# Kernel tuning notes

Measured on AMD Instinct MI355X. Metric: run time of the kernel, lower is better.

The kernel has to match this reference:

```python
import jax, jax.numpy as jnp
import numpy as np

N = 50000
E = 800000
D = 128          # in_dim = hid_dim = out_dim
R = 8            # num_rels
B = 8            # num_bases
N_LAYERS = 2


def _rgcn_conv(x, basis, comp, root, bias, src, dst, etype):
    """One PyG-style RGCNConv with basis decomposition, mean aggregation per
    relation, root (self-loop) weight and bias.
    x: [N, Din]; basis: [B, Din, Dout]; comp: [R, B]; root: [Din, Dout]; bias: [Dout].
    """
    n = x.shape[0]
    # Relation weights from basis decomposition: W[r] = sum_b comp[r,b] * basis[b]
    W = jnp.einsum('rb,bio->rio', comp, basis)           # [R, Din, Dout]
    # Transform every node under every relation, then gather per-edge message.
    H = jnp.einsum('ni,rio->nro', x, W)                  # [N, R, Dout]
    msg = H[src, etype]                                  # [E, Dout]
    # Per-(dst, relation) in-degree for mean aggregation (PyG aggr='mean').
    deg = jnp.zeros((n, R), x.dtype).at[dst, etype].add(1.0)
    inv = 1.0 / jnp.maximum(deg[dst, etype], 1.0)        # [E]
    agg = jnp.zeros((n, W.shape[2]), x.dtype).at[dst].add(msg * inv[:, None])
    return agg + x @ root + bias


def setup_inputs() -> dict:
    key = jax.random.key(0)
    ks = jax.random.split(key, 3 + 4 * N_LAYERS)
    x = jax.random.normal(ks[0], (N, D), dtype=jnp.float32)
    edge_index = jax.random.randint(ks[1], (2, E), 0, N, dtype=jnp.int64)
    edge_type = jax.random.randint(ks[2], (E,), 0, R, dtype=jnp.int64)
    inp = {'x': x, 'edge_index': edge_index, 'edge_type': edge_type}
    scale = 1.0 / np.sqrt(D)
    for l in range(N_LAYERS):
        k0, k1, k2 = ks[3 + 4 * l], ks[4 + 4 * l], ks[5 + 4 * l]
        inp[f'basis{l}'] = jax.random.normal(k0, (B, D, D), dtype=jnp.float32) * scale
        inp[f'comp{l}'] = jax.random.normal(k1, (R, B), dtype=jnp.float32) * (1.0 / np.sqrt(B))
        inp[f'root{l}'] = jax.random.normal(k2, (D, D), dtype=jnp.float32) * scale
        inp[f'bias{l}'] = jnp.zeros((D,), dtype=jnp.float32)
    return inp


def reference(x, edge_index, edge_type,
              basis0, comp0, root0, bias0,
              basis1, comp1, root1, bias1):
    src, dst = edge_index[0], edge_index[1]
    etype = edge_type
    h = _rgcn_conv(x, basis0, comp0, root0, bias0, src, dst, etype)
    h = jax.nn.relu(h)                 # activation between layers (dropout=0.0)
    h = _rgcn_conv(h, basis1, comp1, root1, bias1, src, dst, etype)
    return h
```

## Files before the change

### kernel.cpp

```cpp
#include <hip/hip_runtime.h>

#define NN 50000
#define EE 800000
#define DD 128
#define RR 8
#define SLOTS 9
#define KSTACK 1152
#define NR2 (NN * RR)
#define GRPB 32
#define STROW 304
#define STW (GRPB * STROW)

typedef __attribute__((ext_vector_type(8))) short bf16x8;
typedef __attribute__((ext_vector_type(4))) float f32x4;

__device__ inline float bf2f(ushort u) {
    union { uint i; float f; } v; v.i = ((uint)u) << 16; return v.f;
}
__device__ inline ushort f2bf(float f) {
    uint b = __float_as_uint(f);
    uint r = (b + 0x7fffu + ((b >> 16) & 1u)) >> 16;
    return (ushort)r;
}

__global__ void __launch_bounds__(256) k_build_w4(
        const float* __restrict__ b0, const float* __restrict__ c0,
        const float* __restrict__ r0, const float* __restrict__ b1,
        const float* __restrict__ c1, const float* __restrict__ r1,
        ushort* __restrict__ w0, ushort* __restrict__ w1) {
    __shared__ float tile[32][132];
    const float* basis = blockIdx.y ? b1 : b0;
    const float* comp  = blockIdx.y ? c1 : c0;
    const float* root  = blockIdx.y ? r1 : r0;
    ushort* wT         = blockIdx.y ? w1 : w0;
    int tid = threadIdx.x;
    int k0 = blockIdx.x * 32;
    #pragma unroll
    for (int it = 0; it < 16; ++it) {
        int idx = it * 256 + tid;
        int kk = idx >> 7, o = idx & 127;
        int k = k0 + kk;
        float val;
        if (k < RR * DD) {
            int r = k >> 7, i = k & 127;
            float s = 0.f;
            #pragma unroll
            for (int b = 0; b < 8; ++b) s += comp[r * 8 + b] * basis[(b * 128 + i) * 128 + o];
            val = s;
        } else {
            val = root[(k - RR * DD) * 128 + o];
        }
        tile[kk][o] = val;
    }
    __syncthreads();
    int o = tid >> 1, half = tid & 1;
    int s = k0 >> 7, i0 = k0 & 127;
    ushort* wp = wT + ((size_t)(s * 128 + o)) * 128 + i0 + half * 16;
    #pragma unroll
    for (int j = 0; j < 8; ++j) {
        float lo = tile[half * 16 + 2 * j][o];
        float hi = tile[half * 16 + 2 * j + 1][o];
        uint pk;
        asm("v_cvt_pk_bf16_f32 %0, %1, %2" : "=v"(pk) : "v"(lo), "v"(hi));
        *(uint*)(wp + 2 * j) = pk;
    }
}

__global__ void k_hist(const int* __restrict__ ei, const int* __restrict__ et,
                       int* __restrict__ deg_dr, int* __restrict__ row_cnt) {
    int e = blockIdx.x * 256 + threadIdx.x;
    if (e < EE) {
        int d = ei[EE + e], t = et[e];
        atomicAdd(&deg_dr[d * RR + t], 1);
        atomicAdd(&row_cnt[d], 1);
    }
}

__global__ void k_scan1(const int* __restrict__ cnt, int* __restrict__ bsum, int n) {
    __shared__ int s[256];
    int t = threadIdx.x;
    int i = blockIdx.x * 256 + t;
    s[t] = (i < n) ? cnt[i] : 0;
    __syncthreads();
    for (int o = 128; o > 0; o >>= 1) {
        if (t < o) s[t] += s[t + o];
        __syncthreads();
    }
    if (t == 0) bsum[blockIdx.x] = s[0];
}

__global__ void k_scan2(int* __restrict__ bsum, int nb) {
    __shared__ int s[256];
    int t = threadIdx.x;
    int v = (t < nb) ? bsum[t] : 0;
    s[t] = v;
    __syncthreads();
    for (int o = 1; o < 256; o <<= 1) {
        int u = (t >= o) ? s[t - o] : 0;
        __syncthreads();
        s[t] += u;
        __syncthreads();
    }
    if (t < nb) bsum[t] = s[t] - v;
}

__global__ void k_scan3(const int* __restrict__ cnt, const int* __restrict__ boff,
                        int* __restrict__ ptr, int n) {
    __shared__ int s[256];
    int t = threadIdx.x;
    int i = blockIdx.x * 256 + t;
    int v = (i < n) ? cnt[i] : 0;
    s[t] = v;
    __syncthreads();
    for (int o = 1; o < 256; o <<= 1) {
        int u = (t >= o) ? s[t - o] : 0;
        __syncthreads();
        s[t] += u;
        __syncthreads();
    }
    if (i < n) ptr[i + 1] = boff[blockIdx.x] + s[t];
    if (i == 0) ptr[0] = 0;
}

__global__ void k_scatter(const int* __restrict__ ei, const int* __restrict__ et,
                          const int* __restrict__ row_ptr, const int* __restrict__ deg_dr,
                          int* __restrict__ cursor, int2* __restrict__ ekw) {
    int e = blockIdx.x * 256 + threadIdx.x;
    if (e < EE) {
        int s = ei[e], d = ei[EE + e], t = et[e];
        int p = row_ptr[d] + atomicAdd(&cursor[d], 1);
        int2 pk;
        pk.x = s * SLOTS + t;
        pk.y = __float_as_int(1.f / (float)deg_dr[d * RR + t]);
        ekw[p] = pk;
    }
}

__global__ void __launch_bounds__(512, 2) k_gemmH3(
        const float* __restrict__ Af32, const ushort* __restrict__ Abf,
        const ushort* __restrict__ BT, ushort* __restrict__ H) {
    __shared__ char lds[8 * STW];
    char* atb = lds;
    int tid = threadIdx.x, wid = tid >> 6, lane = tid & 63;
    int blockrow = blockIdx.x * GRPB;

    {
        int row = tid >> 4, seg = tid & 15;
        int gr = blockrow + row; if (gr > NN - 1) gr = NN - 1;
        uint4 pk;
        if (Af32) {
            const float4* sp = (const float4*)(Af32 + (size_t)gr * DD + seg * 8);
            float4 v0 = sp[0], v1 = sp[1];
            asm("v_cvt_pk_bf16_f32 %0, %1, %2" : "=v"(pk.x) : "v"(v0.x), "v"(v0.y));
            asm("v_cvt_pk_bf16_f32 %0, %1, %2" : "=v"(pk.y) : "v"(v0.z), "v"(v0.w));
            asm("v_cvt_pk_bf16_f32 %0, %1, %2" : "=v"(pk.z) : "v"(v1.x), "v"(v1.y));
            asm("v_cvt_pk_bf16_f32 %0, %1, %2" : "=v"(pk.w) : "v"(v1.z), "v"(v1.w));
        } else {
            pk = *(const uint4*)(Abf + (size_t)gr * DD + seg * 8);
        }
        uint off = (uint)(row * 256) + (((uint)seg * 16) ^ ((uint)(row & 7) << 4));
        *(uint4*)(atb + off) = pk;
    }
    __syncthreads();

    int rlo = lane & 15, q = lane >> 4;
    int colw = wid * 144;
    f32x4 acc[2][9];
    #pragma unroll
    for (int f = 0; f < 2; ++f)
        #pragma unroll
        for (int c = 0; c < 9; ++c) acc[f][c] = (f32x4){0.f, 0.f, 0.f, 0.f};

    const ushort* bp = BT + (size_t)(colw + rlo) * DD + q * 8;
    uint x7 = (uint)(rlo & 7) << 4;
    #pragma unroll
    for (int kk = 0; kk < 4; ++kk) {
        uint loff = ((uint)(kk * 64 + q * 16)) ^ x7;
        bf16x8 a0 = *(const bf16x8*)(atb + rlo * 256 + loff);
        bf16x8 a1 = *(const bf16x8*)(atb + (rlo + 16) * 256 + loff);
        #pragma unroll
        for (int c = 0; c < 9; ++c) {
            bf16x8 b = *(const bf16x8*)(bp + (size_t)c * 16 * DD + kk * 32);
            acc[0][c] = __builtin_amdgcn_mfma_f32_16x16x32_bf16(a0, b, acc[0][c], 0, 0, 0);
            acc[1][c] = __builtin_amdgcn_mfma_f32_16x16x32_bf16(a1, b, acc[1][c], 0, 0, 0);
        }
    }
    __syncthreads();

    char* stb = lds + wid * STW;
    #pragma unroll
    for (int f = 0; f < 2; ++f) {
        #pragma unroll
        for (int c = 0; c < 9; ++c) {
            #pragma unroll
            for (int rg = 0; rg < 4; ++rg) {
                int r = f * 16 + q * 4 + rg;
                *(ushort*)(stb + r * STROW + (c * 16 + rlo) * 2) = f2bf(acc[f][c][rg]);
            }
        }
    }
    #pragma unroll
    for (int k = 0; k < 9; ++k) {
        int ci = k * 64 + lane;
        int r = (int)(((uint)ci * 58255u) >> 20);
        int j = ci - r * 18;
        int row = blockrow + r;
        if (row < NN) {
            uint4 v = *(const uint4*)(stb + r * STROW + j * 16);
            *(uint4*)(H + (size_t)row * KSTACK + colw + j * 8) = v;
        }
    }
}

__global__ void __launch_bounds__(256) k_agg2(const ushort* __restrict__ H,
                                              const int* __restrict__ row_ptr,
                                              const int2* __restrict__ ekw,
                                              const float* __restrict__ bias,
                                              ushort* __restrict__ hout,
                                              float* __restrict__ fout) {
    int wid = threadIdx.x >> 6, lane = threadIdx.x & 63;
    int n = blockIdx.x * 4 + wid;
    int l2 = lane << 1;
    uint su = *(const uint*)(H + ((size_t)n * SLOTS + RR) * DD + l2);
    float a0 = bf2f((ushort)(su & 0xffffu));
    float a1 = bf2f((ushort)(su >> 16));
    int p = row_ptr[n], p1 = row_ptr[n + 1];
    for (; p + 4 <= p1; p += 4) {
        int2 e0 = ekw[p], e1 = ekw[p + 1], e2 = ekw[p + 2], e3 = ekw[p + 3];
        uint u0 = *(const uint*)(H + (size_t)e0.x * DD + l2);
        uint u1 = *(const uint*)(H + (size_t)e1.x * DD + l2);
        uint u2 = *(const uint*)(H + (size_t)e2.x * DD + l2);
        uint u3 = *(const uint*)(H + (size_t)e3.x * DD + l2);
        float w0 = __int_as_float(e0.y), w1 = __int_as_float(e1.y);
        float w2 = __int_as_float(e2.y), w3 = __int_as_float(e3.y);
        a0 += w0 * bf2f((ushort)(u0 & 0xffffu)) + w1 * bf2f((ushort)(u1 & 0xffffu))
            + w2 * bf2f((ushort)(u2 & 0xffffu)) + w3 * bf2f((ushort)(u3 & 0xffffu));
        a1 += w0 * bf2f((ushort)(u0 >> 16)) + w1 * bf2f((ushort)(u1 >> 16))
            + w2 * bf2f((ushort)(u2 >> 16)) + w3 * bf2f((ushort)(u3 >> 16));
    }
    for (; p < p1; ++p) {
        int2 e = ekw[p];
        uint u = *(const uint*)(H + (size_t)e.x * DD + l2);
        float w = __int_as_float(e.y);
        a0 += w * bf2f((ushort)(u & 0xffffu));
        a1 += w * bf2f((ushort)(u >> 16));
    }
    a0 += bias[l2];
    a1 += bias[l2 + 1];
    if (hout) {
        a0 = fmaxf(a0, 0.f);
        a1 = fmaxf(a1, 0.f);
        *(uint*)(hout + (size_t)n * DD + l2) = (uint)f2bf(a0) | ((uint)f2bf(a1) << 16);
    } else {
        float2 v; v.x = a0; v.y = a1;
        *(float2*)(fout + (size_t)n * DD + l2) = v;
    }
}

extern "C" void kernel_launch(void* const* d_in, const int* in_sizes, int n_in,
                              void* d_out, int out_size, void* d_ws, size_t ws_size,
                              hipStream_t stream) {
    const float* x      = (const float*)d_in[0];
    const int*   ei     = (const int*)d_in[1];
    const int*   et     = (const int*)d_in[2];
    const float* basis0 = (const float*)d_in[3];
    const float* comp0  = (const float*)d_in[4];
    const float* root0  = (const float*)d_in[5];
    const float* bias0  = (const float*)d_in[6];
    const float* basis1 = (const float*)d_in[7];
    const float* comp1  = (const float*)d_in[8];
    const float* root1  = (const float*)d_in[9];
    const float* bias1  = (const float*)d_in[10];
    float* out = (float*)d_out;

    char* ws = (char*)d_ws;
    size_t off = 0;
    auto alloc = [&](size_t bytes) -> void* {
        void* p = ws + off;
        off += (bytes + 255) & ~(size_t)255;
        return p;
    };
    int*    deg_dr  = (int*)alloc((size_t)NR2 * 4);
    int*    row_cnt = (int*)alloc((size_t)NN * 4);
    int*    cursor  = (int*)alloc((size_t)NN * 4);
    size_t zero_bytes = off;
    int*    row_ptr = (int*)alloc((size_t)(NN + 1) * 4);
    int*    bsum    = (int*)alloc(256 * 4);
    int2*   ekw     = (int2*)alloc((size_t)EE * 8);
    ushort* BT0     = (ushort*)alloc((size_t)KSTACK * DD * 2);
    ushort* BT1     = (ushort*)alloc((size_t)KSTACK * DD * 2);
    ushort* h       = (ushort*)alloc((size_t)NN * DD * 2);
    ushort* H       = (ushort*)alloc((size_t)NN * KSTACK * 2);
    if (off > ws_size) return;

    hipMemsetAsync(d_ws, 0, zero_bytes, stream);

    dim3 wgrid(KSTACK / 32, 2);
    k_build_w4<<<wgrid, 256, 0, stream>>>(basis0, comp0, root0, basis1, comp1, root1, BT0, BT1);
    k_hist<<<3125, 256, 0, stream>>>(ei, et, deg_dr, row_cnt);
    k_scan1<<<196, 256, 0, stream>>>(row_cnt, bsum, NN);
    k_scan2<<<1, 256, 0, stream>>>(bsum, 196);
    k_scan3<<<196, 256, 0, stream>>>(row_cnt, bsum, row_ptr, NN);
    k_scatter<<<3125, 256, 0, stream>>>(ei, et, row_ptr, deg_dr, cursor, ekw);

    int ggrid = (NN + GRPB - 1) / GRPB;
    k_gemmH3<<<ggrid, 512, 0, stream>>>(x, nullptr, BT0, H);
    k_agg2<<<12500, 256, 0, stream>>>(H, row_ptr, ekw, bias0, h, nullptr);
    k_gemmH3<<<ggrid, 512, 0, stream>>>(nullptr, h, BT1, H);
    k_agg2<<<12500, 256, 0, stream>>>(H, row_ptr, ekw, bias1, nullptr, out);
}
```

Baseline: 363.9 us.

## Split H GEMM into smaller 16-row, half-column blocks with 2D grid

The node-transform GEMM now handles 16 rows per block instead of 32 and splits the 1152 output columns across a second grid dimension. Each block has 256 threads, and each wave computes one 16-row MFMA fragment over 144 columns. This halves the accumulator registers and shared memory per block, which allows more resident blocks and a finer grid. The cost is that each B-matrix fragment is reused across fewer rows, so weight traffic from cache goes up. The input row clamp and the output bounds check are removed because 50000 divides evenly by 16.

```diff
diff --git a/kernel.cpp b/kernel.cpp
--- a/kernel.cpp
+++ b/kernel.cpp
@@ -7,7 +7,7 @@
 #define SLOTS 9
 #define KSTACK 1152
 #define NR2 (NN * RR)
-#define GRPB 32
+#define GRPB 16
 #define STROW 304
 #define STW (GRPB * STROW)
 
@@ -136,17 +136,18 @@
     }
 }
 
-__global__ void __launch_bounds__(512, 2) k_gemmH3(
+__global__ void __launch_bounds__(256, 4) k_gemmH4(
         const float* __restrict__ Af32, const ushort* __restrict__ Abf,
         const ushort* __restrict__ BT, ushort* __restrict__ H) {
-    __shared__ char lds[8 * STW];
+    __shared__ char lds[4 * STW];
     char* atb = lds;
     int tid = threadIdx.x, wid = tid >> 6, lane = tid & 63;
     int blockrow = blockIdx.x * GRPB;
+    int colbase = blockIdx.y * 576 + wid * 144;
 
     {
         int row = tid >> 4, seg = tid & 15;
-        int gr = blockrow + row; if (gr > NN - 1) gr = NN - 1;
+        int gr = blockrow + row;
         uint4 pk;
         if (Af32) {
             const float4* sp = (const float4*)(Af32 + (size_t)gr * DD + seg * 8);
@@ -164,50 +165,41 @@
     __syncthreads();
 
     int rlo = lane & 15, q = lane >> 4;
-    int colw = wid * 144;
-    f32x4 acc[2][9];
-    #pragma unroll
-    for (int f = 0; f < 2; ++f)
-        #pragma unroll
-        for (int c = 0; c < 9; ++c) acc[f][c] = (f32x4){0.f, 0.f, 0.f, 0.f};
-
-    const ushort* bp = BT + (size_t)(colw + rlo) * DD + q * 8;
+    f32x4 acc[9];
+    #pragma unroll
+    for (int c = 0; c < 9; ++c) acc[c] = (f32x4){0.f, 0.f, 0.f, 0.f};
+
+    const ushort* bp = BT + (size_t)(colbase + rlo) * DD + q * 8;
     uint x7 = (uint)(rlo & 7) << 4;
     #pragma unroll
     for (int kk = 0; kk < 4; ++kk) {
         uint loff = ((uint)(kk * 64 + q * 16)) ^ x7;
-        bf16x8 a0 = *(const bf16x8*)(atb + rlo * 256 + loff);
-        bf16x8 a1 = *(const bf16x8*)(atb + (rlo + 16) * 256 + loff);
+        bf16x8 a = *(const bf16x8*)(atb + rlo * 256 + loff);
         #pragma unroll
         for (int c = 0; c < 9; ++c) {
             bf16x8 b = *(const bf16x8*)(bp + (size_t)c * 16 * DD + kk * 32);
-            acc[0][c] = __builtin_amdgcn_mfma_f32_16x16x32_bf16(a0, b, acc[0][c], 0, 0, 0);
-            acc[1][c] = __builtin_amdgcn_mfma_f32_16x16x32_bf16(a1, b, acc[1][c], 0, 0, 0);
+            acc[c] = __builtin_amdgcn_mfma_f32_16x16x32_bf16(a, b, acc[c], 0, 0, 0);
         }
     }
     __syncthreads();
 
     char* stb = lds + wid * STW;
     #pragma unroll
-    for (int f = 0; f < 2; ++f) {
+    for (int c = 0; c < 9; ++c) {
         #pragma unroll
-        for (int c = 0; c < 9; ++c) {
-            #pragma unroll
-            for (int rg = 0; rg < 4; ++rg) {
-                int r = f * 16 + q * 4 + rg;
-                *(ushort*)(stb + r * STROW + (c * 16 + rlo) * 2) = f2bf(acc[f][c][rg]);
-            }
-        }
-    }
-    #pragma unroll
-    for (int k = 0; k < 9; ++k) {
+        for (int rg = 0; rg < 4; ++rg) {
+            int r = q * 4 + rg;
+            *(ushort*)(stb + r * STROW + (c * 16 + rlo) * 2) = f2bf(acc[c][rg]);
+        }
+    }
+    #pragma unroll
+    for (int k = 0; k < 5; ++k) {
         int ci = k * 64 + lane;
-        int r = (int)(((uint)ci * 58255u) >> 20);
-        int j = ci - r * 18;
-        int row = blockrow + r;
-        if (row < NN) {
+        if (ci < 288) {
+            int r = (int)(((uint)ci * 58255u) >> 20);
+            int j = ci - r * 18;
             uint4 v = *(const uint4*)(stb + r * STROW + j * 16);
-            *(uint4*)(H + (size_t)row * KSTACK + colw + j * 8) = v;
+            *(uint4*)(H + (size_t)(blockrow + r) * KSTACK + colbase + j * 8) = v;
         }
     }
 }
@@ -303,9 +295,9 @@
     k_scan3<<<196, 256, 0, stream>>>(row_cnt, bsum, row_ptr, NN);
     k_scatter<<<3125, 256, 0, stream>>>(ei, et, row_ptr, deg_dr, cursor, ekw);
 
-    int ggrid = (NN + GRPB - 1) / GRPB;
-    k_gemmH3<<<ggrid, 512, 0, stream>>>(x, nullptr, BT0, H);
+    dim3 ggrid(NN / GRPB, 2);
+    k_gemmH4<<<ggrid, 256, 0, stream>>>(x, nullptr, BT0, H);
     k_agg2<<<12500, 256, 0, stream>>>(H, row_ptr, ekw, bias0, h, nullptr);
-    k_gemmH3<<<ggrid, 512, 0, stream>>>(nullptr, h, BT1, H);
+    k_gemmH4<<<ggrid, 256, 0, stream>>>(nullptr, h, BT1, H);
     k_agg2<<<12500, 256, 0, stream>>>(H, row_ptr, ekw, bias1, nullptr, out);
 }
```

After: 429.7 us. +18.1%, slower.
